# Optimization experiments

Hardware: AMD Instinct MI355X
Metric: run time of the kernel (lower is better)

The kernel has to match this reference:

```python
import jax, jax.numpy as jnp
import numpy as np

N_FFT = 2048
HOP = 512
SR = 48000
T = 2_880_000  # 60 s stereo @ 48 kHz, multiple of HOP


def _hann(n):
    # torch.hann_window default (periodic=True)
    return (0.5 - 0.5 * jnp.cos(2.0 * jnp.pi * jnp.arange(n) / n)).astype(jnp.float32)


def _stft(x, win):
    # x: [C, T] -> [C, F, bins] complex64 (torch.stft center=True, reflect pad)
    pad = N_FFT // 2
    xp = jnp.pad(x, ((0, 0), (pad, pad)), mode='reflect')
    n_frames = 1 + (xp.shape[-1] - N_FFT) // HOP
    idx = jnp.arange(n_frames)[:, None] * HOP + jnp.arange(N_FFT)[None, :]
    frames = xp[:, idx] * win  # [C, F, N_FFT]
    return jnp.fft.rfft(frames, axis=-1)


def _istft(S, win, length):
    # S: [C, F, bins] -> [C, length]; overlap-add with window-square normalization
    frames = jnp.fft.irfft(S, n=N_FFT, axis=-1) * win  # [C, F, N_FFT]
    nF = frames.shape[1]
    total = (nF - 1) * HOP + N_FFT
    idx = jnp.arange(nF)[:, None] * HOP + jnp.arange(N_FFT)[None, :]
    ola = jnp.zeros((frames.shape[0], total), frames.dtype).at[:, idx].add(frames)
    wsum = jnp.zeros((total,), win.dtype).at[idx].add(jnp.broadcast_to(win ** 2, idx.shape))
    out = ola / jnp.where(wsum > 1e-11, wsum, 1.0)
    pad = N_FFT // 2
    return out[:, pad:pad + length]


def _eq_band(audio, freq, gain_db, q=1.0):
    win = _hann(N_FFT)
    S = _stft(audio, win)  # [C, F, bins]
    bins = S.shape[-1]
    freqs = jnp.linspace(0.0, 24000.0, bins)
    mask = jnp.exp(-((freqs - freq) / (freq / q)) ** 2)  # [bins]
    g_lin = 10.0 ** (gain_db / 20.0)
    S = S * (1.0 + (g_lin - 1.0) * mask)
    return _istft(S, win, audio.shape[-1])


def _compress(audio, threshold, ratio, attack, release, makeup_gain):
    aa = jnp.abs(audio) + 1e-8
    adb = 20.0 * jnp.log10(aa)
    gr = jnp.maximum(adb - threshold, 0.0) * (1.0 - 1.0 / ratio)  # [C, T]
    a_att = 1.0 - jnp.exp(-1.0 / (attack * SR))
    a_rel = 1.0 - jnp.exp(-1.0 / (release * SR))

    def step(prev, g):
        alpha = jnp.where(g > prev, a_att, a_rel)
        new = (1.0 - alpha) * prev + alpha * g
        return new, new

    init = jnp.zeros((audio.shape[0],), audio.dtype)
    _, gs = jax.lax.scan(step, init, gr[:, 1:].T)  # [T-1, C]
    gain_smooth = jnp.concatenate([init[:, None], gs.T], axis=1)  # [C, T]
    gain_lin = 10.0 ** ((-gain_smooth + makeup_gain) / 20.0)
    return jnp.sign(audio) * aa * gain_lin


def setup_inputs() -> dict:
    key = jax.random.key(0)
    audio = 0.1 * jax.random.normal(key, (2, T), dtype=jnp.float32)
    f32 = lambda v: jnp.float32(v)
    return {
        'audio': audio,
        'eq_low_gain': f32(3.0),
        'eq_low_mid_gain': f32(-2.0),
        'eq_high_mid_gain': f32(2.5),
        'eq_high_gain': f32(1.5),
        'comp_threshold': f32(-18.0),
        'comp_ratio': f32(4.0),
        'comp_attack': f32(0.01),
        'comp_release': f32(0.1),
        'comp_makeup_gain': f32(3.0),
        'saturation': f32(1.5),
    }


def reference(audio, eq_low_gain, eq_low_mid_gain, eq_high_mid_gain, eq_high_gain,
              comp_threshold, comp_ratio, comp_attack, comp_release,
              comp_makeup_gain, saturation):
    x = _eq_band(audio, 100.0, eq_low_gain)
    x = _eq_band(x, 500.0, eq_low_mid_gain)
    x = _eq_band(x, 3000.0, eq_high_mid_gain)
    x = _eq_band(x, 10000.0, eq_high_gain)
    x = _compress(x, comp_threshold, comp_ratio, comp_attack, comp_release, comp_makeup_gain)
    # saturation branch (original: python if on .item(); here jnp.where)
    return jnp.where(saturation > 1.0, jnp.tanh(x * saturation) / saturation, x)
```

## Files before the change

### kernel.cpp

```cpp
#include <hip/hip_runtime.h>
#include <math.h>

#define T_LEN   2880000
#define LASTFR  5625
#define NBLK_EQ 625
#define SEG     7680
#define NSEG    375
#define KREC    15
#define NREC    512
#define PROWS   528
#define RST     384
#define PL      (PROWS * RST)
#define SPL     (NREC * RST)

typedef float2 c2;
__device__ __forceinline__ c2 cadd(c2 a, c2 b){ return make_float2(a.x+b.x, a.y+b.y); }
__device__ __forceinline__ c2 csub(c2 a, c2 b){ return make_float2(a.x-b.x, a.y-b.y); }
__device__ __forceinline__ c2 cmul(c2 a, c2 b){ return make_float2(a.x*b.x - a.y*b.y, a.x*b.y + a.y*b.x); }
__device__ __forceinline__ c2 cmulj(c2 a, c2 b){ return make_float2(a.x*b.x + a.y*b.y, a.y*b.x - a.x*b.y); }

template<int SGN>
__device__ __forceinline__ void dft8(c2 v[8]) {
    const float r = 0.70710678118654752f;
    c2 t0 = cadd(v[0], v[4]), t1 = csub(v[0], v[4]);
    c2 t2 = cadd(v[2], v[6]), t3 = csub(v[2], v[6]);
    c2 u0 = cadd(v[1], v[5]), u1 = csub(v[1], v[5]);
    c2 u2 = cadd(v[3], v[7]), u3 = csub(v[3], v[7]);
    c2 t3r = (SGN < 0) ? make_float2(t3.y, -t3.x) : make_float2(-t3.y, t3.x);
    c2 u3r = (SGN < 0) ? make_float2(u3.y, -u3.x) : make_float2(-u3.y, u3.x);
    c2 E0 = cadd(t0, t2), E2 = csub(t0, t2);
    c2 E1 = cadd(t1, t3r), E3 = csub(t1, t3r);
    c2 O0 = cadd(u0, u2), O2 = csub(u0, u2);
    c2 O1 = cadd(u1, u3r), O3 = csub(u1, u3r);
    c2 O1w = (SGN < 0) ? make_float2(r*(O1.x+O1.y), r*(O1.y-O1.x))
                       : make_float2(r*(O1.x-O1.y), r*(O1.x+O1.y));
    c2 O2w = (SGN < 0) ? make_float2(O2.y, -O2.x) : make_float2(-O2.y, O2.x);
    c2 O3w = (SGN < 0) ? make_float2(r*(O3.y-O3.x), -r*(O3.x+O3.y))
                       : make_float2(-r*(O3.x+O3.y), r*(O3.x-O3.y));
    v[0] = cadd(E0, O0);  v[4] = csub(E0, O0);
    v[1] = cadd(E1, O1w); v[5] = csub(E1, O1w);
    v[2] = cadd(E2, O2w); v[6] = csub(E2, O2w);
    v[3] = cadd(E3, O3w); v[7] = csub(E3, O3w);
}

__device__ __forceinline__ c2 shx(c2 v, int m) {
    return make_float2(__shfl_xor(v.x, m), __shfl_xor(v.y, m));
}

__device__ __forceinline__ void emit_chunk(float* __restrict__ dst, const float* __restrict__ WN,
                                           int cchunk, int tid, c2 r0, c2 r1) {
    const bool edge = (cchunk <= 2) || (cchunk >= 5626);
    #pragma unroll
    for (int q = 0; q < 2; ++q) {
        c2 rr = (q == 0) ? r0 : r1;
        int m = cchunk * 512 + (q << 8) + tid;
        float inv = 0.66666666666667f;
        if (edge) {
            int tmn = (m >= 2048) ? (((m - 2048) >> 9) + 1) : 0;
            int tmx = min(LASTFR, m >> 9);
            float wsum = 0.0f;
            for (int tt = tmn; tt <= tmx; ++tt) {
                float w = WN[m - (tt << 9)];
                wsum += w * w;
            }
            inv = (wsum > 1e-11f) ? (1.0f / wsum) : 1.0f;
        }
        int o = m - 1024;
        dst[o]         = rr.x * inv;
        dst[T_LEN + o] = rr.y * inv;
    }
}

__global__ __launch_bounds__(256) void eq_band_kernel(
    const float* __restrict__ src, float* __restrict__ dst,
    const float* __restrict__ gain_db_p, const float f0)
{
    __shared__ c2 SA[2048];
    __shared__ c2 TWs1[2048];
    __shared__ c2 TWs2[256];
    __shared__ c2 TWs3[32];
    __shared__ float MKs[2048];
    __shared__ float WN[2048];

    const int tid = threadIdx.x;
    const int b   = blockIdx.x;

    const float gdb   = *gain_db_p;
    const float g_lin = exp2f(gdb * 0.16609640474436813f);
    const float gm1   = g_lin - 1.0f;

    const float st2048 = 6.283185307179586f / 2048.0f;
    for (int idx = tid; idx < 2048; idx += 256) {
        int m = idx >> 8, j = idx & 255;
        float ang = st2048 * (float)(j * m);
        TWs1[idx] = make_float2(cosf(ang), -sinf(ang));
        WN[idx] = 0.5f - 0.5f * cosf(st2048 * (float)idx);
        int tt = idx & 255;
        int bb = tt >> 2, jj = tt & 3;
        int qrev = ((jj & 1) << 1) | (jj >> 1);
        int k = (bb >> 3) + ((bb & 7) << 3) + (m << 6) + (qrev << 9);
        int kk = (k > 1024) ? (2048 - k) : k;
        float f = (float)kk * (24000.0f / 1024.0f);
        float d = (f - f0) / f0;
        MKs[idx] = (1.0f + gm1 * expf(-d * d)) * (1.0f / 2048.0f);
    }
    {
        int m = tid >> 5, j2 = tid & 31;
        float ang = (6.283185307179586f / 256.0f) * (float)(j2 * m);
        TWs2[tid] = make_float2(cosf(ang), -sinf(ang));
    }
    if (tid < 32) {
        int m = tid >> 2, j = tid & 3;
        float ang = (6.283185307179586f / 32.0f) * (float)(j * m);
        TWs3[tid] = make_float2(cosf(ang), -sinf(ang));
    }
    __syncthreads();

    const int t0   = max(0, 9 * b - 1);
    const int t1   = min(LASTFR, 9 * b + 10);
    const int cmin = 9 * b + 2;
    const int cmax = 9 * b + 10;

    c2 ring[8];
    #pragma unroll
    for (int q = 0; q < 8; ++q) ring[q] = make_float2(0.0f, 0.0f);

    for (int t = t0; t <= t1; ++t) {
        for (int j = tid; j < 2048; j += 256) {
            int ss = t * 512 + j - 1024;
            ss = (ss < 0) ? -ss : ss;
            ss = (ss >= T_LEN) ? (2 * T_LEN - 2 - ss) : ss;
            float w = WN[j];
            SA[j] = make_float2(src[ss] * w, src[T_LEN + ss] * w);
        }
        __syncthreads();

        c2 v[8];

        #pragma unroll
        for (int k = 0; k < 8; ++k) v[k] = SA[tid + (k << 8)];
        dft8<-1>(v);
        #pragma unroll
        for (int m = 1; m < 8; ++m) v[m] = cmul(v[m], TWs1[(m << 8) + tid]);
        #pragma unroll
        for (int m = 0; m < 8; ++m) SA[tid + (m << 8)] = v[m];
        __syncthreads();

        {
            int c = tid >> 5, j2 = tid & 31;
            int base = (c << 8) + j2;
            #pragma unroll
            for (int k = 0; k < 8; ++k) v[k] = SA[base + (k << 5)];
            dft8<-1>(v);
            #pragma unroll
            for (int m = 1; m < 8; ++m) v[m] = cmul(v[m], TWs2[(m << 5) + j2]);
            __syncthreads();
            #pragma unroll
            for (int m = 0; m < 8; ++m) SA[(c << 8) + (m << 5) + (j2 ^ (m << 2))] = v[m];
        }
        __syncthreads();

        {
            int bb = tid >> 2, j = tid & 3;
            int base = bb << 5, bx = (bb & 7) << 2;
            #pragma unroll
            for (int k = 0; k < 8; ++k) v[k] = SA[base + ((k << 2) ^ bx) + j];
            dft8<-1>(v);
            #pragma unroll
            for (int m = 1; m < 8; ++m) v[m] = cmul(v[m], TWs3[(m << 2) + j]);
            #pragma unroll
            for (int m = 0; m < 8; ++m) {
                c2 w = v[m];
                c2 p = shx(w, 2);
                c2 e  = (j & 2) ? csub(p, w) : cadd(w, p);
                c2 qq = shx(e, 1);
                c2 lo = (j & 1) ? csub(qq, e) : cadd(e, qq);
                c2 hi = (j & 1) ? make_float2(qq.x - e.y, qq.y + e.x)
                                : make_float2(e.x + qq.y, e.y - qq.x);
                w = (j & 2) ? hi : lo;
                float mk = MKs[(m << 8) + tid];
                w.x *= mk; w.y *= mk;
                c2 p2 = shx(w, 1);
                c2 e2 = (j & 1) ? csub(p2, w) : cadd(w, p2);
                c2 q2 = shx(e2, 2);
                c2 lo2 = (j & 1) ? make_float2(e2.x - q2.y, e2.y + q2.x)
                                 : cadd(e2, q2);
                c2 hi2 = (j & 1) ? make_float2(q2.x + e2.y, q2.y - e2.x)
                                 : csub(q2, e2);
                v[m] = (j & 2) ? hi2 : lo2;
            }
            #pragma unroll
            for (int m = 1; m < 8; ++m) v[m] = cmulj(v[m], TWs3[(m << 2) + j]);
            dft8<+1>(v);
            __syncthreads();
            #pragma unroll
            for (int k = 0; k < 8; ++k) SA[base + ((k << 2) ^ bx) + j] = v[k];
        }
        __syncthreads();

        {
            int c = tid >> 5, j2 = tid & 31;
            #pragma unroll
            for (int m = 0; m < 8; ++m) v[m] = SA[(c << 8) + (m << 5) + (j2 ^ (m << 2))];
            #pragma unroll
            for (int m = 1; m < 8; ++m) v[m] = cmulj(v[m], TWs2[(m << 5) + j2]);
            dft8<+1>(v);
            __syncthreads();
            #pragma unroll
            for (int k = 0; k < 8; ++k) SA[(c << 8) + (k << 5) + j2] = v[k];
        }
        __syncthreads();

        {
            #pragma unroll
            for (int m = 0; m < 8; ++m) v[m] = SA[tid + (m << 8)];
            #pragma unroll
            for (int m = 1; m < 8; ++m) v[m] = cmulj(v[m], TWs1[(m << 8) + tid]);
            dft8<+1>(v);
            #pragma unroll
            for (int k = 0; k < 8; ++k) {
                float w = WN[tid + (k << 8)];
                ring[k].x += v[k].x * w;
                ring[k].y += v[k].y * w;
            }
        }
        __syncthreads();

        if (t >= cmin) emit_chunk(dst, WN, t, tid, ring[0], ring[1]);
        #pragma unroll
        for (int q = 0; q < 6; ++q) ring[q] = ring[q + 2];
        ring[6] = make_float2(0.0f, 0.0f);
        ring[7] = make_float2(0.0f, 0.0f);
    }
    for (int c = t1 + 1; c <= cmax; ++c) {
        emit_chunk(dst, WN, c, tid, ring[0], ring[1]);
        #pragma unroll
        for (int q = 0; q < 6; ++q) ring[q] = ring[q + 2];
        ring[6] = make_float2(0.0f, 0.0f);
        ring[7] = make_float2(0.0f, 0.0f);
    }
}

__device__ __forceinline__ float gaval(float v, float thr, float coef) {
    float aa = fabsf(v) + 1e-8f;
    return fmaxf(6.020599913279624f * __log2f(aa) - thr, 0.0f) * coef;
}

__global__ __launch_bounds__(256) void rec15_kernel(
    const float* __restrict__ y, float4* __restrict__ rec,
    const float* __restrict__ thr_p, const float* __restrict__ ratio_p,
    const float* __restrict__ att_p, const float* __restrict__ rel_p)
{
    __shared__ float4 Lsub[32][9][4];
    const int r0 = blockIdx.x * 32;
    const int s0 = blockIdx.y * 64;
    const int c  = blockIdx.z;
    const int tid = threadIdx.x;

    float thr = *thr_p, ratio = *ratio_p;
    float A  = expf(-1.0f / ((*att_p) * 48000.0f));
    float Bc = expf(-1.0f / ((*rel_p) * 48000.0f));
    float ra = (1.0f - Bc) / (1.0f - A);
    float coef = (1.0f - 1.0f / ratio) * (1.0f - A);

    const int rr = tid & 31, cg = tid >> 5;
    const int orow = tid >> 3, oc8 = tid & 7;

    #pragma unroll 1
    for (int it = 0; it < 8; ++it) {
        int s = s0 + it * 8 + cg;
        if (s < NSEG) {
            int r = r0 + rr;
            int li = s * SEG + KREC * r;
            const float* yp = y + (long)c * T_LEN + li;
            float I[16];
            float a = gaval(yp[0], thr, coef);
            if (li == 0) a = 0.0f;
            I[0] = a; I[1] = ra * a;
            #pragma unroll
            for (int n = 1; n < KREC; ++n) {
                a = gaval(yp[n], thr, coef);
                float b = ra * a;
                I[n + 1] = fmaf(Bc, I[n], b);
                #pragma unroll
                for (int j = n; j >= 1; --j)
                    I[j] = fmaxf(fmaf(A, I[j], a), fmaf(Bc, I[j - 1], b));
                I[0] = fmaf(A, I[0], a);
            }
            Lsub[rr][cg][0] = make_float4(I[0],  I[1],  I[2],  I[3]);
            Lsub[rr][cg][1] = make_float4(I[4],  I[5],  I[6],  I[7]);
            Lsub[rr][cg][2] = make_float4(I[8],  I[9],  I[10], I[11]);
            Lsub[rr][cg][3] = make_float4(I[12], I[13], I[14], I[15]);
        }
        __syncthreads();
        int so = s0 + it * 8 + oc8;
        if (so < NSEG) {
            #pragma unroll
            for (int q = 0; q < 4; ++q)
                rec[(long)(c * 4 + q) * PL + (r0 + orow) * RST + 4 + so]
                    = Lsub[orow][oc8][q];
        }
        __syncthreads();
    }
}

__global__ __launch_bounds__(256) void padzero_kernel(float4* __restrict__ rec)
{
    int idx = blockIdx.x * 256 + threadIdx.x;
    if (idx >= 8 * NREC * 4) return;
    int colp  = idx & 3;
    int r     = (idx >> 2) & (NREC - 1);
    int plane = idx >> 11;
    rec[(long)plane * PL + r * RST + colp] = make_float4(0.f, 0.f, 0.f, 0.f);
}

struct Rec { float4 a, b, c, d; };

__device__ __forceinline__ void load8(Rec (&bb)[8],
    const float4* p0, const float4* p1, const float4* p2, const float4* p3, int r)
{
    #pragma unroll
    for (int k = 0; k < 8; ++k) {
        int o = (r + k) * RST;
        bb[k].a = p0[o]; bb[k].b = p1[o]; bb[k].c = p2[o]; bb[k].d = p3[o];
    }
}

template<bool STORE>
__device__ __forceinline__ void consume8(Rec (&bb)[8], float* sp, int r, float& p,
                                         const float (&S)[16])
{
    #pragma unroll
    for (int k = 0; k < 8; ++k) {
        Rec v = bb[k];
        float m0 = fmaxf(fmaf(S[0],  p, v.a.x), fmaf(S[1],  p, v.a.y));
        float m1 = fmaxf(fmaf(S[2],  p, v.a.z), fmaf(S[3],  p, v.a.w));
        float m2 = fmaxf(fmaf(S[4],  p, v.b.x), fmaf(S[5],  p, v.b.y));
        float m3 = fmaxf(fmaf(S[6],  p, v.b.z), fmaf(S[7],  p, v.b.w));
        float m4 = fmaxf(fmaf(S[8],  p, v.c.x), fmaf(S[9],  p, v.c.y));
        float m5 = fmaxf(fmaf(S[10], p, v.c.z), fmaf(S[11], p, v.c.w));
        float m6 = fmaxf(fmaf(S[12], p, v.d.x), fmaf(S[13], p, v.d.y));
        float m7 = fmaxf(fmaf(S[14], p, v.d.z), fmaf(S[15], p, v.d.w));
        m0 = fmaxf(m0, m1); m2 = fmaxf(m2, m3);
        m4 = fmaxf(m4, m5); m6 = fmaxf(m6, m7);
        m0 = fmaxf(m0, m2); m4 = fmaxf(m4, m6);
        p = fmaxf(m0, m4);
        if (STORE) sp[(r + k) * RST] = p;
    }
}

template<bool STORE>
__device__ void scan_pass(const float4* p0, const float4* p1, const float4* p2,
                          const float4* p3, float* sp, float& p, const float (&S)[16])
{
    Rec bA[8], bB[8];
    load8(bA, p0, p1, p2, p3, 0);
    __builtin_amdgcn_sched_barrier(0);
    int r = 0;
    #pragma unroll 1
    for (int gg = 0; gg < NREC / 16; ++gg) {
        load8(bB, p0, p1, p2, p3, r + 8);
        __builtin_amdgcn_sched_barrier(0);
        consume8<STORE>(bA, sp, r, p, S);
        __builtin_amdgcn_sched_barrier(0);
        load8(bA, p0, p1, p2, p3, r + 16);
        __builtin_amdgcn_sched_barrier(0);
        consume8<STORE>(bB, sp, r + 8, p, S);
        __builtin_amdgcn_sched_barrier(0);
        r += 16;
    }
}

__global__ __launch_bounds__(64, 1) void scan_kernel(
    const float4* __restrict__ rec, float* __restrict__ gsP,
    const float* __restrict__ att_p, const float* __restrict__ rel_p)
{
    int gid = blockIdx.x * 64 + threadIdx.x;
    int g2 = min(gid, 2 * NSEG - 1);
    int c = g2 / NSEG;
    int s = g2 - c * NSEG;

    float A  = expf(-1.0f / ((*att_p) * 48000.0f));
    float Bc = expf(-1.0f / ((*rel_p) * 48000.0f));
    float S[16];
    {
        float pa = 1.0f;
        #pragma unroll
        for (int j = 15; j >= 0; --j) { S[j] = pa; pa *= A; }
        float pb = 1.0f;
        #pragma unroll
        for (int j = 0; j < 16; ++j) { S[j] *= pb; pb *= Bc; }
    }

    float* sbase = gsP + (long)c * SPL + 4 + s;
    float p = 0.0f;

    #pragma unroll 1
    for (int j = 0; j < 4; ++j) {
        const float4* p0 = rec + (long)(c * 4 + 0) * PL + s + j;
        const float4* p1 = rec + (long)(c * 4 + 1) * PL + s + j;
        const float4* p2 = rec + (long)(c * 4 + 2) * PL + s + j;
        const float4* p3 = rec + (long)(c * 4 + 3) * PL + s + j;
        scan_pass<false>(p0, p1, p2, p3, nullptr, p, S);
    }
    {
        const float4* p0 = rec + (long)(c * 4 + 0) * PL + s + 4;
        const float4* p1 = rec + (long)(c * 4 + 1) * PL + s + 4;
        const float4* p2 = rec + (long)(c * 4 + 2) * PL + s + 4;
        const float4* p3 = rec + (long)(c * 4 + 3) * PL + s + 4;
        scan_pass<true>(p0, p1, p2, p3, sbase, p, S);
    }
}

__global__ __launch_bounds__(256) void final_kernel(
    const float* __restrict__ y, const float* __restrict__ gsP, float* __restrict__ out,
    const float* __restrict__ thr_p, const float* __restrict__ ratio_p,
    const float* __restrict__ att_p, const float* __restrict__ rel_p,
    const float* __restrict__ mk_p, const float* __restrict__ sat_p)
{
    __shared__ float LP[64][34];
    const int r0 = blockIdx.x * 32;
    const int s0 = blockIdx.y * 64;
    const int c  = blockIdx.z;
    const int tid = threadIdx.x;

    float thr = *thr_p, ratio = *ratio_p, mk = *mk_p, sat = *sat_p;
    float A  = expf(-1.0f / ((*att_p) * 48000.0f));
    float Bc = expf(-1.0f / ((*rel_p) * 48000.0f));
    float ra = (1.0f - Bc) / (1.0f - A);
    float coef = (1.0f - 1.0f / ratio) * (1.0f - A);
    const float* gb = gsP + (long)c * SPL;

    for (int idx = tid; idx < 33 * 64; idx += 256) {
        int rr = idx >> 6, ss = idx & 63;
        int s = s0 + ss;
        float v = 0.0f;
        if (s < NSEG) {
            int row = r0 - 1 + rr;
            if (row >= 0)      v = gb[row * RST + 4 + s];
            else if (s > 0)    v = gb[(NREC - 1) * RST + 4 + s - 1];
        }
        LP[ss][rr] = v;
    }
    __syncthreads();

    #pragma unroll 1
    for (int it = 0; it < 8; ++it) {
        int idx = it * 256 + tid;
        int ss = idx >> 5, rr = idx & 31;
        int s = s0 + ss;
        if (s >= NSEG) continue;
        int r = r0 + rr;
        int li = s * SEG + KREC * r;
        const float* yp = y + (long)c * T_LEN + li;
        float* op = out + (long)c * T_LEN + li;
        float p = LP[ss][rr];
        #pragma unroll
        for (int q = 0; q < KREC; ++q) {
            float v = yp[q];
            float a = gaval(v, thr, coef);
            if (li + q == 0) a = 0.0f;
            p = fmaxf(fmaf(A, p, a), fmaf(Bc, p, ra * a));
            float aa = fabsf(v) + 1e-8f;
            float gl = exp2f((mk - p) * 0.16609640474436813f);
            float ro = aa * gl;
            ro = (v < 0.0f) ? -ro : ro;
            if (sat > 1.0f) ro = tanhf(ro * sat) / sat;
            op[q] = ro;
        }
    }
}

extern "C" void kernel_launch(void* const* d_in, const int* in_sizes, int n_in,
                              void* d_out, int out_size, void* d_ws, size_t ws_size,
                              hipStream_t stream)
{
    const float* audio = (const float*)d_in[0];
    const float* g1    = (const float*)d_in[1];
    const float* g2    = (const float*)d_in[2];
    const float* g3    = (const float*)d_in[3];
    const float* g4    = (const float*)d_in[4];
    const float* thr   = (const float*)d_in[5];
    const float* ratio = (const float*)d_in[6];
    const float* att   = (const float*)d_in[7];
    const float* rel   = (const float*)d_in[8];
    const float* mkup  = (const float*)d_in[9];
    const float* sat   = (const float*)d_in[10];

    float* out  = (float*)d_out;
    float* bufA = (float*)d_ws;
    float4* rec = (float4*)(bufA + 2 * T_LEN);
    float*  gsP = (float*)(rec + 8 * (long)PL);

    eq_band_kernel<<<NBLK_EQ, 256, 0, stream>>>(audio, out,  g1, 100.0f);
    eq_band_kernel<<<NBLK_EQ, 256, 0, stream>>>(out,   bufA, g2, 500.0f);
    eq_band_kernel<<<NBLK_EQ, 256, 0, stream>>>(bufA,  out,  g3, 3000.0f);
    eq_band_kernel<<<NBLK_EQ, 256, 0, stream>>>(out,   bufA, g4, 10000.0f);

    padzero_kernel<<<(8 * NREC * 4 + 255) / 256, 256, 0, stream>>>(rec);
    dim3 tgrid(NREC / 32, (NSEG + 63) / 64, 2);
    rec15_kernel<<<tgrid, 256, 0, stream>>>(bufA, rec, thr, ratio, att, rel);
    scan_kernel<<<12, 64, 0, stream>>>(rec, gsP, att, rel);
    final_kernel<<<tgrid, 256, 0, stream>>>(bufA, gsP, out,
                                            thr, ratio, att, rel, mkup, sat);
}
```

Measured before the change: 767.0 us.

## Replace shifted-window scan passes with iterative end-state handoff kernels

The scan previously ran four warm-up passes over shifted column windows, using zero-padded lead columns, before the storing pass. It now runs separate kernel launches in which each segment's warm-up starts from the previous segment's end state, written by the prior launch to a small buffer, so the padzero kernel is removed. This adds four kernel launches and relies on the recurrence converging after a fixed number of iterations. Total scan work stays about the same.

```diff
diff --git a/kernel.cpp b/kernel.cpp
--- a/kernel.cpp
+++ b/kernel.cpp
@@ -304,15 +304,6 @@
     }
 }
 
-__global__ __launch_bounds__(256) void padzero_kernel(float4* __restrict__ rec)
-{
-    int idx = blockIdx.x * 256 + threadIdx.x;
-    if (idx >= 8 * NREC * 4) return;
-    int colp  = idx & 3;
-    int r     = (idx >> 2) & (NREC - 1);
-    int plane = idx >> 11;
-    rec[(long)plane * PL + r * RST + colp] = make_float4(0.f, 0.f, 0.f, 0.f);
-}
 
 struct Rec { float4 a, b, c, d; };
 
@@ -371,8 +362,10 @@
     }
 }
 
-__global__ __launch_bounds__(64, 1) void scan_kernel(
+template<int MODE>
+__global__ __launch_bounds__(64, 1) void scan_iter_kernel(
     const float4* __restrict__ rec, float* __restrict__ gsP,
+    const float* __restrict__ eIn, float* __restrict__ eOut,
     const float* __restrict__ att_p, const float* __restrict__ rel_p)
 {
     int gid = blockIdx.x * 64 + threadIdx.x;
@@ -392,23 +385,20 @@
         for (int j = 0; j < 16; ++j) { S[j] *= pb; pb *= Bc; }
     }
 
-    float* sbase = gsP + (long)c * SPL + 4 + s;
     float p = 0.0f;
-
-    #pragma unroll 1
-    for (int j = 0; j < 4; ++j) {
-        const float4* p0 = rec + (long)(c * 4 + 0) * PL + s + j;
-        const float4* p1 = rec + (long)(c * 4 + 1) * PL + s + j;
-        const float4* p2 = rec + (long)(c * 4 + 2) * PL + s + j;
-        const float4* p3 = rec + (long)(c * 4 + 3) * PL + s + j;
+    if (MODE != 0) p = (s == 0) ? 0.0f : eIn[c * NSEG + s - 1];
+
+    const float4* p0 = rec + (long)(c * 4 + 0) * PL + 4 + s;
+    const float4* p1 = rec + (long)(c * 4 + 1) * PL + 4 + s;
+    const float4* p2 = rec + (long)(c * 4 + 2) * PL + 4 + s;
+    const float4* p3 = rec + (long)(c * 4 + 3) * PL + 4 + s;
+
+    if (MODE == 2) {
+        float* sbase = gsP + (long)c * SPL + 4 + s;
+        scan_pass<true>(p0, p1, p2, p3, sbase, p, S);
+    } else {
         scan_pass<false>(p0, p1, p2, p3, nullptr, p, S);
-    }
-    {
-        const float4* p0 = rec + (long)(c * 4 + 0) * PL + s + 4;
-        const float4* p1 = rec + (long)(c * 4 + 1) * PL + s + 4;
-        const float4* p2 = rec + (long)(c * 4 + 2) * PL + s + 4;
-        const float4* p3 = rec + (long)(c * 4 + 3) * PL + s + 4;
-        scan_pass<true>(p0, p1, p2, p3, sbase, p, S);
+        eOut[c * NSEG + s] = p;
     }
 }
 
@@ -491,16 +481,23 @@
     float* bufA = (float*)d_ws;
     float4* rec = (float4*)(bufA + 2 * T_LEN);
     float*  gsP = (float*)(rec + 8 * (long)PL);
+    float*  eA  = gsP + 2 * (long)SPL;
+    float*  eB  = eA + 2 * NSEG;
 
     eq_band_kernel<<<NBLK_EQ, 256, 0, stream>>>(audio, out,  g1, 100.0f);
     eq_band_kernel<<<NBLK_EQ, 256, 0, stream>>>(out,   bufA, g2, 500.0f);
     eq_band_kernel<<<NBLK_EQ, 256, 0, stream>>>(bufA,  out,  g3, 3000.0f);
     eq_band_kernel<<<NBLK_EQ, 256, 0, stream>>>(out,   bufA, g4, 10000.0f);
 
-    padzero_kernel<<<(8 * NREC * 4 + 255) / 256, 256, 0, stream>>>(rec);
     dim3 tgrid(NREC / 32, (NSEG + 63) / 64, 2);
     rec15_kernel<<<tgrid, 256, 0, stream>>>(bufA, rec, thr, ratio, att, rel);
-    scan_kernel<<<12, 64, 0, stream>>>(rec, gsP, att, rel);
+
+    scan_iter_kernel<0><<<12, 64, 0, stream>>>(rec, gsP, nullptr, eA, att, rel);
+    scan_iter_kernel<1><<<12, 64, 0, stream>>>(rec, gsP, eA, eB, att, rel);
+    scan_iter_kernel<1><<<12, 64, 0, stream>>>(rec, gsP, eB, eA, att, rel);
+    scan_iter_kernel<1><<<12, 64, 0, stream>>>(rec, gsP, eA, eB, att, rel);
+    scan_iter_kernel<2><<<12, 64, 0, stream>>>(rec, gsP, eB, nullptr, att, rel);
+
     final_kernel<<<tgrid, 256, 0, stream>>>(bufA, gsP, out,
                                             thr, ratio, att, rel, mkup, sat);
 }
```

New measurement: 770.0 us. No clear change (+0.4%).
